# Performance work log

Hardware: AMD Instinct MI355X
Metric: run time of the kernel (lower is better)

Reference implementation:

```python
import jax, jax.numpy as jnp
import numpy as np

N_HEAD = 8


def setup_inputs() -> dict:
    key = jax.random.key(0)
    k1, k2, k3 = jax.random.split(key, 3)
    B, D, L = 4, 1024, 2048  # channels-first: (batch, feature, seq)
    q = jax.random.normal(k1, (B, D, L), dtype=jnp.float32)
    k = jax.random.normal(k2, (B, D, L), dtype=jnp.float32)
    v = jax.random.normal(k3, (B, D, L), dtype=jnp.float32)
    gamma = jnp.ones((), dtype=jnp.float32)  # nn.Parameter scalar, init 1.0
    return {"q": q, "k": k, "v": v, "gamma": gamma}


def reference(q, k, v, gamma):
    # q, k, v: (B, D, L) channels-first. Head split on feature dim (-2).
    B, Dq, Lq = q.shape
    Dv, Lk = v.shape[-2], v.shape[-1]
    h = N_HEAD
    dq = Dq // h  # per-head query/key dim
    dv = Dv // h  # per-head value dim
    qh = q.reshape(B, h, dq, Lq)
    kh = k.reshape(B, h, dq, Lk)
    vh = v.reshape(B, h, dv, Lk)
    # scale = sqrt(q.size(-2)) AFTER head split, i.e. sqrt(d_head)
    scale = 1.0 / jnp.sqrt(jnp.asarray(dq, dtype=q.dtype))
    # qk: (B, h, Lq, Lk)
    qk = jnp.einsum('bhdq,bhdl->bhql', qh, kh) * scale
    sm = jax.nn.softmax(qk, axis=-1)
    # torch: (sm.unsqueeze(-3) * v.unsqueeze(-2)).sum(-1) == contraction over Lk
    ret = jnp.einsum('bhql,bhdl->bhdq', sm, vh)  # (B, h, dv, Lq)
    ret = ret.reshape(B, Dv, Lq)  # torch: ret.view(-1, v_shape[-2], q_shape[-1])
    return gamma * ret
```

## Files before the change

### kernel.cpp

```cpp
#include <hip/hip_runtime.h>

#define SEQ 2048
#define DHEAD 128
#define BK 32
#define NBH 32

typedef __attribute__((ext_vector_type(8))) short bf16x8;
typedef __attribute__((ext_vector_type(4))) short bf16x4;
typedef __attribute__((ext_vector_type(16))) float f32x16;
typedef __attribute__((ext_vector_type(4))) unsigned int u32x4;

__device__ __forceinline__ unsigned short f2bf(float f) {
    unsigned u = __builtin_bit_cast(unsigned, f);
    u += 0x7fffu + ((u >> 16) & 1u);
    return (unsigned short)(u >> 16);
}

__device__ __forceinline__ void gload16(const unsigned short* g, unsigned short* l) {
    __builtin_amdgcn_global_load_lds((const __attribute__((address_space(1))) void*)g,
                                     (__attribute__((address_space(3))) void*)l, 16, 0, 0);
}

__global__ __launch_bounds__(256)
void cvt_kernel(const float* __restrict__ kin, const float* __restrict__ vin,
                unsigned short* __restrict__ kout, unsigned short* __restrict__ vout) {
    const int tid = threadIdx.x;
    if (blockIdx.x < 1024) {
        __shared__ unsigned short tileT[DHEAD][66];
        const int bh = blockIdx.x & 31;
        const int l0 = (blockIdx.x >> 5) * 64;
        const float* ip = kin + (size_t)bh * DHEAD * SEQ;
        unsigned short* opx = kout + ((size_t)bh * SEQ + l0) * DHEAD;
        const int l4 = (tid & 15) * 4;
        const int dq = tid >> 4;
        for (int pass = 0; pass < 8; ++pass) {
            int d = pass * 16 + dq;
            float4 f = *(const float4*)&ip[(size_t)d * SEQ + l0 + l4];
            unsigned lo = (unsigned)f2bf(f.x) | ((unsigned)f2bf(f.y) << 16);
            unsigned hi = (unsigned)f2bf(f.z) | ((unsigned)f2bf(f.w) << 16);
            *(unsigned*)&tileT[d][l4]     = lo;
            *(unsigned*)&tileT[d][l4 + 2] = hi;
        }
        __syncthreads();
        const int lw = tid >> 2;
        const int cw = tid & 3;
        for (int j = 0; j < 4; ++j) {
            int pc = j * 4 + cw;
            int lc = pc ^ (lw & 7);
            unsigned short tmp[8];
            for (int k2 = 0; k2 < 8; ++k2) tmp[k2] = tileT[lc * 8 + k2][lw];
            *(bf16x8*)&opx[(size_t)lw * DHEAD + pc * 8] = *(bf16x8*)tmp;
        }
    } else {
        size_t f = ((size_t)(blockIdx.x - 1024) * 256 + tid) * 8;
        int bh  = (int)(f >> 18);
        int rem = (int)(f & 262143);
        int kt  = rem >> 12;
        int r2  = rem & 4095;
        int dv  = r2 >> 5;
        int e0  = r2 & 31;
        const float* src = vin + ((size_t)bh * DHEAD + dv) * SEQ + kt * BK + e0;
        float4 a = *(const float4*)src;
        float4 b = *(const float4*)(src + 4);
        unsigned short p0[4] = {f2bf(a.x), f2bf(a.y), f2bf(a.z), f2bf(a.w)};
        unsigned short p1[4] = {f2bf(b.x), f2bf(b.y), f2bf(b.z), f2bf(b.w)};
        const int aa = e0 >> 4;
        const int bb = (e0 >> 3) & 1;
        const int w  = (dv >> 1) & 3;
        size_t rowb = ((size_t)bh * (SEQ / BK) + kt) * (DHEAD * BK) + (size_t)dv * BK;
        *(bf16x4*)&vout[rowb + (size_t)(((2 * aa) ^ w) * 8 + 4 * bb)]     = *(bf16x4*)p0;
        *(bf16x4*)&vout[rowb + (size_t)(((2 * aa + 1) ^ w) * 8 + 4 * bb)] = *(bf16x4*)p1;
    }
}

__global__ __launch_bounds__(256, 2)
void attn_main(const float* __restrict__ q,
               const unsigned short* __restrict__ kTg,
               const unsigned short* __restrict__ vW,
               const float* __restrict__ gamma,
               float* __restrict__ out) {
    __shared__ __attribute__((aligned(16))) unsigned short kS[2][BK * DHEAD];
    __shared__ __attribute__((aligned(16))) unsigned short vS[2][DHEAD * BK];

    const int tid  = threadIdx.x;
    const int wv   = tid >> 6;
    const int lane = tid & 63;
    const int c5   = lane & 31;
    const int hi   = lane >> 5;

    const int bh  = blockIdx.x & 31;
    const int qlb = blockIdx.x >> 5;
    const size_t base = (size_t)bh * SEQ * DHEAD;

    const float* qp = q + base;
    const unsigned short* kb = kTg + base;
    const unsigned short* vb = vW + base;
    float* op = out + base;

    const int ql = qlb * 128 + wv * 32 + c5;
    const float SCL = 0.08838834764831845f * 1.44269504088896340f;

    gload16(kb + tid * 8,         &kS[0][tid * 8]);
    gload16(kb + (tid + 256) * 8, &kS[0][(tid + 256) * 8]);
    gload16(vb + tid * 8,         &vS[0][tid * 8]);
    gload16(vb + (tid + 256) * 8, &vS[0][(tid + 256) * 8]);

    bf16x8 qf[8];
#pragma unroll
    for (int s = 0; s < 8; ++s) {
        bf16x8 t;
#pragma unroll
        for (int j = 0; j < 8; ++j)
            t[j] = (short)f2bf(qp[(size_t)(s * 16 + hi * 8 + j) * SEQ + ql] * SCL);
        qf[s] = t;
    }

    f32x16 accO[4];
#pragma unroll
    for (int t = 0; t < 4; ++t)
#pragma unroll
        for (int i = 0; i < 16; ++i) accO[t][i] = 0.f;
    float lp = 0.f;

    const int ksw = c5 & 7;
    const int vsw = (c5 >> 1) & 3;

    for (int kt = 0; kt < SEQ / BK; ++kt) {
        const int cur = kt & 1;
        __syncthreads();

        if (kt + 1 < SEQ / BK) {
            const unsigned short* kg = kb + (size_t)(kt + 1) * (BK * DHEAD);
            gload16(kg + tid * 8,         &kS[cur ^ 1][tid * 8]);
            gload16(kg + (tid + 256) * 8, &kS[cur ^ 1][(tid + 256) * 8]);
            const unsigned short* vg = vb + (size_t)(kt + 1) * (DHEAD * BK);
            gload16(vg + tid * 8,         &vS[cur ^ 1][tid * 8]);
            gload16(vg + (tid + 256) * 8, &vS[cur ^ 1][(tid + 256) * 8]);
        }

        bf16x8 kf[8], vf[8];
#pragma unroll
        for (int s = 0; s < 8; ++s)
            kf[s] = *(const bf16x8*)&kS[cur][c5 * DHEAD + (((2 * s + hi) ^ ksw) * 8)];
#pragma unroll
        for (int t = 0; t < 4; ++t)
#pragma unroll
            for (int s2 = 0; s2 < 2; ++s2)
                vf[t * 2 + s2] = *(const bf16x8*)&vS[cur][(32 * t + c5) * BK + (((2 * s2 + hi) ^ vsw) * 8)];

        f32x16 sT;
#pragma unroll
        for (int i = 0; i < 16; ++i) sT[i] = 0.f;
#pragma unroll
        for (int s = 0; s < 8; ++s)
            sT = __builtin_amdgcn_mfma_f32_32x32x16_bf16(kf[s], qf[s], sT, 0, 0, 0);

        unsigned pw[8];
#pragma unroll
        for (int i = 0; i < 8; ++i) {
            float pa = exp2f(sT[2 * i]);
            float pb = exp2f(sT[2 * i + 1]);
            lp += pa + pb;
            unsigned r;
            asm("v_cvt_pk_bf16_f32 %0, %1, %2" : "=v"(r) : "v"(pa), "v"(pb));
            pw[i] = r;
        }
        bf16x8 pf0 = __builtin_bit_cast(bf16x8, (u32x4){pw[0], pw[1], pw[2], pw[3]});
        bf16x8 pf1 = __builtin_bit_cast(bf16x8, (u32x4){pw[4], pw[5], pw[6], pw[7]});

#pragma unroll
        for (int t = 0; t < 4; ++t) {
            accO[t] = __builtin_amdgcn_mfma_f32_32x32x16_bf16(vf[t * 2],     pf0, accO[t], 0, 0, 0);
            accO[t] = __builtin_amdgcn_mfma_f32_32x32x16_bf16(vf[t * 2 + 1], pf1, accO[t], 0, 0, 0);
        }
    }

    const float L = lp + __shfl_xor(lp, 32);
    const float sc = gamma[0] / L;
#pragma unroll
    for (int t = 0; t < 4; ++t)
#pragma unroll
        for (int r = 0; r < 16; ++r) {
            int dvr = 32 * t + (r & 3) + 8 * (r >> 2) + 4 * hi;
            op[(size_t)dvr * SEQ + ql] = accO[t][r] * sc;
        }
}

extern "C" void kernel_launch(void* const* d_in, const int* in_sizes, int n_in,
                              void* d_out, int out_size, void* d_ws, size_t ws_size,
                              hipStream_t stream) {
    (void)in_sizes; (void)n_in; (void)out_size; (void)ws_size;
    const float* q = (const float*)d_in[0];
    const float* k = (const float*)d_in[1];
    const float* v = (const float*)d_in[2];
    const float* g = (const float*)d_in[3];
    float* out = (float*)d_out;

    const size_t PER_T = (size_t)NBH * SEQ * DHEAD;
    unsigned short* kws = (unsigned short*)d_ws;
    unsigned short* vws = kws + PER_T;

    cvt_kernel<<<dim3(1024 + 4096), dim3(256), 0, stream>>>(k, v, kws, vws);
    attn_main<<<dim3(512), dim3(256), 0, stream>>>(q, kws, vws, g, out);
}
```

Baseline: 211.5 us.

## Process two query sub-tiles per wave with 128-thread blocks, reusing K/V fragments

Each wave now handles 64 query columns as two 32-wide sub-tiles, so every K and V fragment read from LDS feeds two MFMAs instead of one. Blocks shrink to 2 waves of 128 threads, keeping 128 queries per block and the same grid. The LDS swizzle patterns for K and V are extended with extra XOR bits in both the convert kernel and the main loop to reduce bank conflicts. The cost is roughly double the accumulator and Q registers per wave and half as many waves per block, which may lower occupancy and latency hiding.

```diff
diff --git a/kernel.cpp b/kernel.cpp
--- a/kernel.cpp
+++ b/kernel.cpp
@@ -44,9 +44,10 @@
         __syncthreads();
         const int lw = tid >> 2;
         const int cw = tid & 3;
+        const int ksw = (lw & 7) ^ (((lw >> 3) & 3) << 1);
         for (int j = 0; j < 4; ++j) {
             int pc = j * 4 + cw;
-            int lc = pc ^ (lw & 7);
+            int lc = pc ^ ksw;
             unsigned short tmp[8];
             for (int k2 = 0; k2 < 8; ++k2) tmp[k2] = tileT[lc * 8 + k2][lw];
             *(bf16x8*)&opx[(size_t)lw * DHEAD + pc * 8] = *(bf16x8*)tmp;
@@ -66,14 +67,14 @@
         unsigned short p1[4] = {f2bf(b.x), f2bf(b.y), f2bf(b.z), f2bf(b.w)};
         const int aa = e0 >> 4;
         const int bb = (e0 >> 3) & 1;
-        const int w  = (dv >> 1) & 3;
+        const int w  = ((dv >> 1) & 3) ^ ((dv >> 3) & 3);
         size_t rowb = ((size_t)bh * (SEQ / BK) + kt) * (DHEAD * BK) + (size_t)dv * BK;
         *(bf16x4*)&vout[rowb + (size_t)(((2 * aa) ^ w) * 8 + 4 * bb)]     = *(bf16x4*)p0;
         *(bf16x4*)&vout[rowb + (size_t)(((2 * aa + 1) ^ w) * 8 + 4 * bb)] = *(bf16x4*)p1;
     }
 }
 
-__global__ __launch_bounds__(256, 2)
+__global__ __launch_bounds__(128, 1)
 void attn_main(const float* __restrict__ q,
                const unsigned short* __restrict__ kTg,
                const unsigned short* __restrict__ vW,
@@ -97,33 +98,38 @@
     const unsigned short* vb = vW + base;
     float* op = out + base;
 
-    const int ql = qlb * 128 + wv * 32 + c5;
+    const int ql0 = qlb * 128 + wv * 64;
     const float SCL = 0.08838834764831845f * 1.44269504088896340f;
 
-    gload16(kb + tid * 8,         &kS[0][tid * 8]);
-    gload16(kb + (tid + 256) * 8, &kS[0][(tid + 256) * 8]);
-    gload16(vb + tid * 8,         &vS[0][tid * 8]);
-    gload16(vb + (tid + 256) * 8, &vS[0][(tid + 256) * 8]);
-
-    bf16x8 qf[8];
+#pragma unroll
+    for (int i = 0; i < 4; ++i) {
+        gload16(kb + (size_t)(tid + i * 128) * 8, &kS[0][(tid + i * 128) * 8]);
+        gload16(vb + (size_t)(tid + i * 128) * 8, &vS[0][(tid + i * 128) * 8]);
+    }
+
+    bf16x8 qf0[8], qf1[8];
 #pragma unroll
     for (int s = 0; s < 8; ++s) {
-        bf16x8 t;
-#pragma unroll
-        for (int j = 0; j < 8; ++j)
-            t[j] = (short)f2bf(qp[(size_t)(s * 16 + hi * 8 + j) * SEQ + ql] * SCL);
-        qf[s] = t;
-    }
-
-    f32x16 accO[4];
+        bf16x8 t0, t1;
+#pragma unroll
+        for (int j = 0; j < 8; ++j) {
+            const size_t drow = (size_t)(s * 16 + hi * 8 + j) * SEQ;
+            t0[j] = (short)f2bf(qp[drow + ql0 + c5] * SCL);
+            t1[j] = (short)f2bf(qp[drow + ql0 + 32 + c5] * SCL);
+        }
+        qf0[s] = t0;
+        qf1[s] = t1;
+    }
+
+    f32x16 acc0[4], acc1[4];
 #pragma unroll
     for (int t = 0; t < 4; ++t)
 #pragma unroll
-        for (int i = 0; i < 16; ++i) accO[t][i] = 0.f;
-    float lp = 0.f;
-
-    const int ksw = c5 & 7;
-    const int vsw = (c5 >> 1) & 3;
+        for (int i = 0; i < 16; ++i) { acc0[t][i] = 0.f; acc1[t][i] = 0.f; }
+    float lp0 = 0.f, lp1 = 0.f;
+
+    const int ksw = (c5 & 7) ^ (((c5 >> 3) & 3) << 1);
+    const int vsw = ((c5 >> 1) & 3) ^ ((c5 >> 3) & 3);
 
     for (int kt = 0; kt < SEQ / BK; ++kt) {
         const int cur = kt & 1;
@@ -131,59 +137,80 @@
 
         if (kt + 1 < SEQ / BK) {
             const unsigned short* kg = kb + (size_t)(kt + 1) * (BK * DHEAD);
-            gload16(kg + tid * 8,         &kS[cur ^ 1][tid * 8]);
-            gload16(kg + (tid + 256) * 8, &kS[cur ^ 1][(tid + 256) * 8]);
             const unsigned short* vg = vb + (size_t)(kt + 1) * (DHEAD * BK);
-            gload16(vg + tid * 8,         &vS[cur ^ 1][tid * 8]);
-            gload16(vg + (tid + 256) * 8, &vS[cur ^ 1][(tid + 256) * 8]);
-        }
-
-        bf16x8 kf[8], vf[8];
-#pragma unroll
-        for (int s = 0; s < 8; ++s)
-            kf[s] = *(const bf16x8*)&kS[cur][c5 * DHEAD + (((2 * s + hi) ^ ksw) * 8)];
+#pragma unroll
+            for (int i = 0; i < 4; ++i) {
+                gload16(kg + (size_t)(tid + i * 128) * 8, &kS[cur ^ 1][(tid + i * 128) * 8]);
+                gload16(vg + (size_t)(tid + i * 128) * 8, &vS[cur ^ 1][(tid + i * 128) * 8]);
+            }
+        }
+
+        f32x16 sT0, sT1;
+#pragma unroll
+        for (int i = 0; i < 16; ++i) { sT0[i] = 0.f; sT1[i] = 0.f; }
+#pragma unroll
+        for (int s = 0; s < 8; ++s) {
+            bf16x8 kf = *(const bf16x8*)&kS[cur][c5 * DHEAD + (((2 * s + hi) ^ ksw) * 8)];
+            sT0 = __builtin_amdgcn_mfma_f32_32x32x16_bf16(kf, qf0[s], sT0, 0, 0, 0);
+            sT1 = __builtin_amdgcn_mfma_f32_32x32x16_bf16(kf, qf1[s], sT1, 0, 0, 0);
+        }
+
+        unsigned pw0[8], pw1[8];
+#pragma unroll
+        for (int i = 0; i < 8; ++i) {
+            float a0 = exp2f(sT0[2 * i]);
+            float b0 = exp2f(sT0[2 * i + 1]);
+            float a1 = exp2f(sT1[2 * i]);
+            float b1 = exp2f(sT1[2 * i + 1]);
+            lp0 += a0 + b0;
+            lp1 += a1 + b1;
+            unsigned r0, r1;
+            asm("v_cvt_pk_bf16_f32 %0, %1, %2" : "=v"(r0) : "v"(a0), "v"(b0));
+            asm("v_cvt_pk_bf16_f32 %0, %1, %2" : "=v"(r1) : "v"(a1), "v"(b1));
+            pw0[i] = r0;
+            pw1[i] = r1;
+        }
+        bf16x8 p0a = __builtin_bit_cast(bf16x8, (u32x4){pw0[0], pw0[1], pw0[2], pw0[3]});
+        bf16x8 p0b = __builtin_bit_cast(bf16x8, (u32x4){pw0[4], pw0[5], pw0[6], pw0[7]});
+        bf16x8 p1a = __builtin_bit_cast(bf16x8, (u32x4){pw1[0], pw1[1], pw1[2], pw1[3]});
+        bf16x8 p1b = __builtin_bit_cast(bf16x8, (u32x4){pw1[4], pw1[5], pw1[6], pw1[7]});
+
+#pragma unroll
+        for (int t = 0; t < 4; ++t) {
+            bf16x8 va = *(const bf16x8*)&vS[cur][(32 * t + c5) * BK + (((0 + hi) ^ vsw) * 8)];
+            bf16x8 vb8 = *(const bf16x8*)&vS[cur][(32 * t + c5) * BK + (((2 + hi) ^ vsw) * 8)];
+            acc0[t] = __builtin_amdgcn_mfma_f32_32x32x16_bf16(va,  p0a, acc0[t], 0, 0, 0);
+            acc0[t] = __builtin_amdgcn_mfma_f32_32x32x16_bf16(vb8, p0b, acc0[t], 0, 0, 0);
+            acc1[t] = __builtin_amdgcn_mfma_f32_32x32x16_bf16(va,  p1a, acc1[t], 0, 0, 0);
+            acc1[t] = __builtin_amdgcn_mfma_f32_32x32x16_bf16(vb8, p1b, acc1[t], 0, 0, 0);
+        }
+    }
+
+    const float gm = gamma[0];
+    {
+        const float L0 = lp0 + __shfl_xor(lp0, 32);
+        const float sc0 = gm / L0;
+        const int ql = ql0 + c5;
 #pragma unroll
         for (int t = 0; t < 4; ++t)
 #pragma unroll
-            for (int s2 = 0; s2 < 2; ++s2)
-                vf[t * 2 + s2] = *(const bf16x8*)&vS[cur][(32 * t + c5) * BK + (((2 * s2 + hi) ^ vsw) * 8)];
-
-        f32x16 sT;
-#pragma unroll
-        for (int i = 0; i < 16; ++i) sT[i] = 0.f;
-#pragma unroll
-        for (int s = 0; s < 8; ++s)
-            sT = __builtin_amdgcn_mfma_f32_32x32x16_bf16(kf[s], qf[s], sT, 0, 0, 0);
-
-        unsigned pw[8];
-#pragma unroll
-        for (int i = 0; i < 8; ++i) {
-            float pa = exp2f(sT[2 * i]);
-            float pb = exp2f(sT[2 * i + 1]);
-            lp += pa + pb;
-            unsigned r;
-            asm("v_cvt_pk_bf16_f32 %0, %1, %2" : "=v"(r) : "v"(pa), "v"(pb));
-            pw[i] = r;
-        }
-        bf16x8 pf0 = __builtin_bit_cast(bf16x8, (u32x4){pw[0], pw[1], pw[2], pw[3]});
-        bf16x8 pf1 = __builtin_bit_cast(bf16x8, (u32x4){pw[4], pw[5], pw[6], pw[7]});
-
-#pragma unroll
-        for (int t = 0; t < 4; ++t) {
-            accO[t] = __builtin_amdgcn_mfma_f32_32x32x16_bf16(vf[t * 2],     pf0, accO[t], 0, 0, 0);
-            accO[t] = __builtin_amdgcn_mfma_f32_32x32x16_bf16(vf[t * 2 + 1], pf1, accO[t], 0, 0, 0);
-        }
-    }
-
-    const float L = lp + __shfl_xor(lp, 32);
-    const float sc = gamma[0] / L;
-#pragma unroll
-    for (int t = 0; t < 4; ++t)
-#pragma unroll
-        for (int r = 0; r < 16; ++r) {
-            int dvr = 32 * t + (r & 3) + 8 * (r >> 2) + 4 * hi;
-            op[(size_t)dvr * SEQ + ql] = accO[t][r] * sc;
-        }
+            for (int r = 0; r < 16; ++r) {
+                int dvr = 32 * t + (r & 3) + 8 * (r >> 2) + 4 * hi;
+                op[(size_t)dvr * SEQ + ql] = acc0[t][r] * sc0;
+            }
+    }
+    {
+        const float L1 = lp1 + __shfl_xor(lp1, 32);
+        const float sc1 = gm / L1;
+        const int ql = ql0 + 32 + c5;
+#pragma unroll
+        for (int t = 0; t < 4; ++t)
+#pragma unroll
+            for (int r = 0; r < 16; ++r) {
+                int dvr = 32 * t + (r & 3) + 8 * (r >> 2) + 4 * hi;
+                op[(size_t)dvr * SEQ + ql] = acc1[t][r] * sc1;
+            }
+    }
 }
 
 extern "C" void kernel_launch(void* const* d_in, const int* in_sizes, int n_in,
@@ -201,5 +228,5 @@
     unsigned short* vws = kws + PER_T;
 
     cvt_kernel<<<dim3(1024 + 4096), dim3(256), 0, stream>>>(k, v, kws, vws);
-    attn_main<<<dim3(512), dim3(256), 0, stream>>>(q, kws, vws, g, out);
-}
+    attn_main<<<dim3(512), dim3(128), 0, stream>>>(q, kws, vws, g, out);
+}
```

Result: slower. 254.6 us (+20.4%).
